# Optimization experiments

Measured on AMD Instinct MI355X. Metric: run time of the kernel, lower is better.

The kernel has to match this reference:

```python
import jax, jax.numpy as jnp
import numpy as np

# Model hyperparameters (match init_kwargs)
B, N_TOK, DIM = 32, 1024, 512
H_GRID, W_GRID = 32, 32
NT = 400
NUM_HEADS, KEY_DIM, ATTN_RATIO = 8, 64, 4
D_V = ATTN_RATIO * KEY_DIM          # 256, per-head value dim
DH = D_V * NUM_HEADS                # 2048
NH_KD = KEY_DIM * NUM_HEADS         # 512
H_KV = DH + NH_KD                   # 2560, kv projection width
NUM_OFFSETS = 100 * 100             # unique (|dx|,|dy|) offsets on 100x100 grid
EPS = 1e-5


def linear_bn(x, w, gamma, beta, mean, var):
    # Linear (no bias) followed by BatchNorm1d in inference form.
    y = x @ w
    return (y - mean) * (gamma * jax.lax.rsqrt(var + EPS)) + beta


def bias_idxs(H, W, nt):
    # attention_offsets[(a,b)] == a*100 + b (order of first-p1 sweep in __init__).
    # query n -> grid point (n//W, n%W); text token t -> (t//100, t%100).
    n = np.arange(H * W)
    i, j = n // W, n % W
    t = np.arange(nt)
    a, b = t // 100, t % 100
    return jnp.asarray(np.abs(i[:, None] - a[None, :]) * 100
                       + np.abs(j[:, None] - b[None, :]))  # (N, NT) int


def setup_inputs() -> dict:
    key = jax.random.key(0)
    ks = jax.random.split(key, 18)
    rn = jax.random.normal
    ru = jax.random.uniform
    return {
        "x": rn(ks[0], (B, N_TOK, DIM), jnp.float32),
        "text": rn(ks[1], (NT, DIM), jnp.float32),
        "q_w": rn(ks[2], (DIM, NH_KD), jnp.float32) * 0.02,
        "q_gamma": ru(ks[3], (NH_KD,), jnp.float32, 0.5, 1.5),
        "q_beta": rn(ks[4], (NH_KD,), jnp.float32) * 0.02,
        "q_mean": rn(ks[5], (NH_KD,), jnp.float32) * 0.02,
        "q_var": ru(ks[6], (NH_KD,), jnp.float32, 0.5, 1.5),
        "kv_w": rn(ks[7], (DIM, H_KV), jnp.float32) * 0.02,
        "kv_gamma": ru(ks[8], (H_KV,), jnp.float32, 0.5, 1.5),
        "kv_beta": rn(ks[9], (H_KV,), jnp.float32) * 0.02,
        "kv_mean": rn(ks[10], (H_KV,), jnp.float32) * 0.02,
        "kv_var": ru(ks[11], (H_KV,), jnp.float32, 0.5, 1.5),
        "proj_w": rn(ks[12], (DH, DIM), jnp.float32) * 0.02,
        "proj_gamma": ru(ks[13], (DIM,), jnp.float32, 0.5, 1.5),
        "proj_beta": rn(ks[14], (DIM,), jnp.float32) * 0.02,
        "proj_mean": rn(ks[15], (DIM,), jnp.float32) * 0.02,
        "proj_var": ru(ks[16], (DIM,), jnp.float32, 0.5, 1.5),
        "attention_biases": rn(ks[17], (NUM_HEADS, NUM_OFFSETS), jnp.float32) * 0.02,
        "H": H_GRID,
        "W": W_GRID,
    }


def reference(x, text, q_w, q_gamma, q_beta, q_mean, q_var,
              kv_w, kv_gamma, kv_beta, kv_mean, kv_var,
              proj_w, proj_gamma, proj_beta, proj_mean, proj_var,
              attention_biases, H, W):
    b, n, _ = x.shape
    nt = text.shape[0]
    scale = KEY_DIM ** -0.5

    # q: (B, heads, N, key_dim)
    q = linear_bn(x, q_w, q_gamma, q_beta, q_mean, q_var)
    q = q.reshape(b, n, NUM_HEADS, KEY_DIM).transpose(0, 2, 1, 3)

    # kv computed once on text, shared across batch: (NT, heads, key_dim + d)
    kv = linear_bn(text, kv_w, kv_gamma, kv_beta, kv_mean, kv_var)
    kv = kv.reshape(nt, NUM_HEADS, KEY_DIM + D_V)
    k, v = kv[:, :, :KEY_DIM], kv[:, :, KEY_DIM:]

    # gathered relative position bias: (heads, N, NT)
    idxs = bias_idxs(H, W, nt)
    bias = attention_biases[:, idxs]

    scores = jnp.einsum('bhnk,thk->bhnt', q, k) * scale + bias
    attn = jax.nn.softmax(scores, axis=-1)

    out = jnp.einsum('bhnt,thd->bhnd', attn, v)          # (B, heads, N, d)
    out = out.transpose(0, 2, 1, 3).reshape(b, n, DH)

    # proj = activation (GELU, exact) -> Linear_BN(dh -> dim)
    out = jax.nn.gelu(out, approximate=False)
    return linear_bn(out, proj_w, proj_gamma, proj_beta, proj_mean, proj_var)
```

## Files before the change

kernel.cpp:

```cpp
#include <hip/hip_runtime.h>
#include <hip/hip_bf16.h>


typedef unsigned short u16;
typedef unsigned int u32;
typedef float  f32x4  __attribute__((ext_vector_type(4)));
typedef float  fl4    __attribute__((ext_vector_type(4)));
typedef short  short8 __attribute__((ext_vector_type(8)));
typedef u32    u32x4  __attribute__((ext_vector_type(4)));
typedef u32    u32x2  __attribute__((ext_vector_type(2)));

#define EPSF 1e-5f
#define NH 8
#define NTP 416
#define LOG2E 1.4426950408889634f
#define QSCALE (0.125f * LOG2E)

static __device__ __forceinline__ u16 f2bf(float f){
  u32 u = __builtin_bit_cast(u32, f);
  u += 0x7FFFu + ((u >> 16) & 1u);
  return (u16)(u >> 16);
}
static __device__ __forceinline__ float u2f(u32 u){
  return __builtin_bit_cast(float, u);
}
static __device__ __forceinline__ u32 pk2bf(float lo, float hi){
  float2 f; f.x = lo; f.y = hi;
  __hip_bfloat162 b = __float22bfloat162_rn(f);
  u32 l = (u32)__bfloat16_as_ushort(b.x);
  u32 h = (u32)__bfloat16_as_ushort(b.y);
  return l | (h << 16);
}
static __device__ __forceinline__ f32x4 mfma16(short8 a, short8 b, f32x4 c){
  return __builtin_amdgcn_mfma_f32_16x16x32_bf16(a, b, c, 0, 0, 0);
}
static __device__ __forceinline__ void gld16(const void* g, void* l){
  __builtin_amdgcn_global_load_lds(
      (const __attribute__((address_space(1))) u32*)g,
      (__attribute__((address_space(3))) u32*)l, 16, 0, 0);
}

__global__ __launch_bounds__(256) void wconv_kernel(
    const float* __restrict__ w, const float* __restrict__ gamma,
    const float* __restrict__ var, u16* __restrict__ wT, int R, int C)
{
  __shared__ u16 tile[64*65];
  const int tx = blockIdx.x, ty = blockIdx.y, tid = threadIdx.x;
  #pragma unroll
  for (int i = 0; i < 16; ++i){
    int lin = tid + i*256;
    int rr = lin >> 6, cc = lin & 63;
    int c = tx*64 + cc;
    float s = gamma[c] * rsqrtf(var[c] + EPSF);
    tile[rr*65 + cc] = f2bf(w[(size_t)(ty*64 + rr)*C + c] * s);
  }
  __syncthreads();
  #pragma unroll
  for (int i = 0; i < 16; ++i){
    int lin = tid + i*256;
    int cc = lin >> 6, rr = lin & 63;
    wT[(size_t)(tx*64 + cc)*R + ty*64 + rr] = tile[rr*65 + cc];
  }
}

__global__ __launch_bounds__(256) void textconv_kernel(
    const float* __restrict__ text, u16* __restrict__ tbf)
{
  int idx = blockIdx.x*256 + threadIdx.x;
  int r = idx >> 9, c = idx & 511;
  float v = (r < 400) ? text[r*512 + c] : 0.f;
  tbf[idx] = f2bf(v);
}

__global__ __launch_bounds__(256) void bias_kernel(
    const float* __restrict__ ab, u16* __restrict__ btab)
{
  int idx = blockIdx.x*256 + threadIdx.x;
  int t = idx % 416;
  int n = (idx / 416) & 1023;
  int h = idx / (416*1024);
  float v;
  if (t >= 400) v = -1e30f;
  else {
    int i = n >> 5, j = n & 31;
    int a = t / 100, bb = t % 100;
    v = ab[h*10000 + abs(i - a)*100 + abs(j - bb)] * LOG2E;
  }
  size_t o = ((size_t)(h*16 + (n >> 6))*13 + (t >> 5))*2048
           + ((n >> 4) & 3)*512 + ((t >> 4) & 1)*256
           + ((t >> 2) & 3)*64 + (n & 15)*4 + (t & 3);
  btab[o] = f2bf(v);
}

template<int MODE, int NXB, int BK>
__global__ __launch_bounds__(256) void gemm_kernel(
    const void* __restrict__ Ap, const u16* __restrict__ BT,
    const float* __restrict__ g1, const float* __restrict__ b1,
    const float* __restrict__ m1, const float* __restrict__ v1,
    void* __restrict__ o0, void* __restrict__ o1, int K, int row_base,
    int rbpx)
{
  __shared__ u16 lds[BK == 64 ? 16384 : 8192];
  constexpr int HALF = (BK == 64) ? 8192 : 4096;
  const int tid = threadIdx.x;
  int cb, rb;
  if (NXB > 0){
    const int L = blockIdx.x;
    const int xcd = L & 7, s = L >> 3;
    cb = s % NXB;
    rb = xcd * rbpx + s / NXB;
  } else {
    cb = blockIdx.x; rb = blockIdx.y;
  }
  const int lane = tid & 63, wid = tid >> 6;
  const int lg = lane >> 4, lc = lane & 15;
  const int wr = wid >> 1, wc = wid & 1;
  const int row0 = rb*128, col0 = cb*128;
  f32x4 acc[4][4] = {};
  const int nkb = K / BK;

  for (int kb = 0; kb < nkb; ++kb){
    if (MODE == 0){
      const float* A = (const float*)Ap;
      #pragma unroll
      for (int it = 0; it < 4; ++it){
        int lin = tid + it*256;
        int row = lin >> 3, c4 = lin & 7;
        const fl4 v = *(const fl4*)(A + (size_t)(row0 + row)*K + kb*32 + c4*4);
        u32x2 p;
        p[0] = pk2bf(v[0], v[1]);
        p[1] = pk2bf(v[2], v[3]);
        *(u32x2*)&lds[row*32 + c4*4] = p;
      }
    } else if (BK == 32){
      const u16* A = (const u16*)Ap;
      #pragma unroll
      for (int it = 0; it < 2; ++it){
        int lin = tid + it*256;
        int row = lin >> 2, seg = lin & 3;
        gld16(A + (size_t)(row0 + row)*K + kb*32 + seg*8, &lds[lin*8]);
      }
    } else {
      const u16* A = (const u16*)Ap;
      #pragma unroll
      for (int it = 0; it < 4; ++it){
        int lin = tid + it*256;
        int row = lin >> 3, seg = lin & 7;
        gld16(A + (size_t)(row0 + row)*K + kb*64 + seg*8, &lds[lin*8]);
      }
    }
    if (BK == 32){
      #pragma unroll
      for (int it = 0; it < 2; ++it){
        int lin = tid + it*256;
        int col = lin >> 2, seg = lin & 3;
        gld16(BT + (size_t)(col0 + col)*K + kb*32 + seg*8, &lds[HALF + lin*8]);
      }
    } else {
      #pragma unroll
      for (int it = 0; it < 4; ++it){
        int lin = tid + it*256;
        int col = lin >> 3, seg = lin & 7;
        gld16(BT + (size_t)(col0 + col)*K + kb*64 + seg*8, &lds[HALF + lin*8]);
      }
    }
    __syncthreads();
    #pragma unroll
    for (int kh = 0; kh < BK/32; ++kh){
      short8 af[4], bfr[4];
      #pragma unroll
      for (int rt = 0; rt < 4; ++rt)
        af[rt] = *(const short8*)&lds[(wr*64 + rt*16 + lc)*BK + kh*32 + lg*8];
      #pragma unroll
      for (int ct = 0; ct < 4; ++ct)
        bfr[ct] = *(const short8*)&lds[HALF + (wc*64 + ct*16 + lc)*BK + kh*32 + lg*8];
      #pragma unroll
      for (int rt = 0; rt < 4; ++rt)
        #pragma unroll
        for (int ct = 0; ct < 4; ++ct)
          acc[rt][ct] = mfma16(af[rt], bfr[ct], acc[rt][ct]);
    }
    __syncthreads();
  }

  if (MODE == 0){
    u16* qws = (u16*)o0;
    #pragma unroll
    for (int ct = 0; ct < 4; ++ct){
      int c = col0 + wc*64 + ct*16 + lc;
      float sc = g1[c] * rsqrtf(v1[c] + EPSF);
      float sh = (b1[c] - m1[c]*sc) * QSCALE;
      int h = c >> 6, dk = c & 63;
      #pragma unroll
      for (int rt = 0; rt < 4; ++rt)
        #pragma unroll
        for (int r = 0; r < 4; ++r){
          int mr = row0 + wr*64 + rt*16 + lg*4 + r;
          int b = mr >> 10, n = mr & 1023;
          qws[(size_t)((b*NH + h)*1024 + n)*64 + dk] =
              f2bf(acc[rt][ct][r]*QSCALE + sh);
        }
    }
  } else if (MODE == 1){
    u16* Kw = (u16*)o0; u16* Vw = (u16*)o1;
    #pragma unroll
    for (int ct = 0; ct < 4; ++ct){
      int c = col0 + wc*64 + ct*16 + lc;
      float sc = g1[c] * rsqrtf(v1[c] + EPSF);
      float sh = b1[c] - m1[c]*sc;
      int h = c / 320, sub = c % 320;
      #pragma unroll
      for (int rt = 0; rt < 4; ++rt)
        #pragma unroll
        for (int r = 0; r < 4; ++r){
          int t = row0 + wr*64 + rt*16 + lg*4 + r;
          if (t < NTP){
            u16 val = f2bf(acc[rt][ct][r] + sh);
            if (sub < 64){
              size_t o = ((size_t)h*13 + (t >> 5))*2048
                       + ((t >> 4) & 1)*1024 + (sub >> 5)*512
                       + ((sub >> 3) & 3)*128 + (t & 15)*8 + (sub & 7);
              Kw[o] = val;
            } else {
              int dv = sub - 64;
              size_t o = ((size_t)h*13 + (t >> 5))*8192
                       + (dv >> 6)*2048 + ((dv >> 4) & 3)*512
                       + ((t >> 3) & 3)*128 + (dv & 15)*8 + (t & 7);
              Vw[o] = val;
            }
          }
        }
    }
  } else {
    float* outp = (float*)o0;
    #pragma unroll
    for (int ct = 0; ct < 4; ++ct){
      int c = col0 + wc*64 + ct*16 + lc;
      float sc = g1[c] * rsqrtf(v1[c] + EPSF);
      float sh = b1[c] - m1[c]*sc;
      #pragma unroll
      for (int rt = 0; rt < 4; ++rt)
        #pragma unroll
        for (int r = 0; r < 4; ++r){
          int mr = row_base + row0 + wr*64 + rt*16 + lg*4 + r;
          outp[(size_t)mr*512 + c] = acc[rt][ct][r] + sh;
        }
    }
  }
}

__global__ __launch_bounds__(256, 3) void attn_kernel(
    const u16* __restrict__ qws, const u16* __restrict__ Kw,
    const u16* __restrict__ Vw, const u16* __restrict__ btab,
    u16* __restrict__ aws, int b_base, int bzbits)
{
  __shared__ char Pb[2][64*80];
  __shared__ float lsum[64];

  const int tid = threadIdx.x;
  const int lane = tid & 63, wid = tid >> 6;
  const int lg = lane >> 4, lc = lane & 15;

  const int L = blockIdx.x;
  const int slot = L >> 3;
  const int bz = slot & ((1 << bzbits) - 1);
  const int qt = slot >> bzbits;
  const int h = L & 7;
  const int b = b_base + bz, n0 = qt*64;

  const u16* qp = qws + ((size_t)((b*NH + h)*1024 + n0 + wid*16 + lc))*64 + lg*8;
  const short8 qf0 = *(const short8*)qp;
  const short8 qf1 = *(const short8*)(qp + 32);

  const u16* kbase = Kw + (size_t)h*13*2048 + lg*128 + lc*8;
  const u16* vbase = Vw + (size_t)h*13*8192 + wid*2048 + lg*128 + lc*8;
  const u16* btb   = btab + ((size_t)(h*16 + qt)*13)*2048 + wid*512 + lg*64 + lc*4;

  float lpart = 0.f;
  f32x4 acc[4][4] = {};
  char* pwr = &Pb[0][0] + (wid*16 + lc)*80 + lg*8;

  short8 kfs[2][4];
  u32x2  bws[2][2];

  kfs[0][0] = *(const short8*)(kbase);
  kfs[0][1] = *(const short8*)(kbase + 512);
  kfs[0][2] = *(const short8*)(kbase + 1024);
  kfs[0][3] = *(const short8*)(kbase + 1536);
  bws[0][0] = *(const u32x2*)(btb);
  bws[0][1] = *(const u32x2*)(btb + 256);

  #pragma unroll
  for (int c = 0; c < 13; ++c){
    const int s = c & 1, ns = (c + 1) & 1;
    const u16* vc = vbase + (size_t)c*8192;
    short8 vf0 = *(const short8*)(vc);
    short8 vf1 = *(const short8*)(vc + 512);
    short8 vf2 = *(const short8*)(vc + 1024);
    short8 vf3 = *(const short8*)(vc + 1536);
    #pragma unroll
    for (int tt = 0; tt < 2; ++tt){
      u32x2 bw = bws[s][tt];
      f32x4 sv;
      sv[0] = u2f(bw[0] << 16); sv[1] = u2f(bw[0] & 0xffff0000u);
      sv[2] = u2f(bw[1] << 16); sv[3] = u2f(bw[1] & 0xffff0000u);
      sv = mfma16(kfs[s][tt*2 + 0], qf0, sv);
      sv = mfma16(kfs[s][tt*2 + 1], qf1, sv);
      float p0 = __builtin_exp2f(sv[0]);
      float p1 = __builtin_exp2f(sv[1]);
      float p2 = __builtin_exp2f(sv[2]);
      float p3 = __builtin_exp2f(sv[3]);
      lpart += (p0 + p1) + (p2 + p3);
      u32x2 pw;
      pw[0] = pk2bf(p0, p1);
      pw[1] = pk2bf(p2, p3);
      *(u32x2*)(pwr + s*5120 + tt*32) = pw;
    }
    if (c < 12){
      const u16* kc = kbase + (size_t)(c + 1)*2048;
      kfs[ns][0] = *(const short8*)(kc);
      kfs[ns][1] = *(const short8*)(kc + 512);
      kfs[ns][2] = *(const short8*)(kc + 1024);
      kfs[ns][3] = *(const short8*)(kc + 1536);
      const u16* bc = btb + (size_t)(c + 1)*2048;
      bws[ns][0] = *(const u32x2*)(bc);
      bws[ns][1] = *(const u32x2*)(bc + 256);
    }
    __syncthreads();
    const char* pb = &Pb[s][0];
    short8 pa[4];
    #pragma unroll
    for (int rt = 0; rt < 4; ++rt)
      pa[rt] = *(const short8*)(pb + (rt*16 + lc)*80 + lg*16);
    __builtin_amdgcn_s_setprio(1);
    #pragma unroll
    for (int rt = 0; rt < 4; ++rt){
      acc[rt][0] = mfma16(pa[rt], vf0, acc[rt][0]);
      acc[rt][1] = mfma16(pa[rt], vf1, acc[rt][1]);
      acc[rt][2] = mfma16(pa[rt], vf2, acc[rt][2]);
      acc[rt][3] = mfma16(pa[rt], vf3, acc[rt][3]);
    }
    __builtin_amdgcn_s_setprio(0);
  }

  lpart += __shfl_xor(lpart, 16);
  lpart += __shfl_xor(lpart, 32);
  if (lane < 16) lsum[wid*16 + lane] = lpart;
  __syncthreads();

  #pragma unroll
  for (int rt = 0; rt < 4; ++rt){
    #pragma unroll
    for (int r = 0; r < 4; ++r){
      const int qrow = rt*16 + lg*4 + r;
      const float linv = __builtin_amdgcn_rcpf(lsum[qrow]);
      const size_t obase = ((size_t)(bz*1024 + n0 + qrow))*2048 + h*256;
      #pragma unroll
      for (int ct = 0; ct < 4; ++ct){
        float x = acc[rt][ct][r] * linv;
        float x2 = x * x;
        float z = x * __builtin_fmaf(0.0356774081f, x2, 0.7978845608f);
        float e = __builtin_exp2f(z * (2.0f * LOG2E));
        float rr = __builtin_amdgcn_rcpf(1.0f + e);
        float g = __builtin_fmaf(-x, rr, x);
        aws[obase + wid*64 + ct*16 + lc] = f2bf(g);
      }
    }
  }
}

extern "C" void kernel_launch(void* const* d_in, const int* in_sizes, int n_in,
                              void* d_out, int out_size, void* d_ws, size_t ws_size,
                              hipStream_t stream)
{
  (void)in_sizes; (void)n_in; (void)out_size;
  const float* x    = (const float*)d_in[0];
  const float* text = (const float*)d_in[1];
  const float* q_w  = (const float*)d_in[2];
  const float* q_g  = (const float*)d_in[3];
  const float* q_b  = (const float*)d_in[4];
  const float* q_m  = (const float*)d_in[5];
  const float* q_v  = (const float*)d_in[6];
  const float* kv_w = (const float*)d_in[7];
  const float* kv_g = (const float*)d_in[8];
  const float* kv_b = (const float*)d_in[9];
  const float* kv_m = (const float*)d_in[10];
  const float* kv_v = (const float*)d_in[11];
  const float* p_w  = (const float*)d_in[12];
  const float* p_g  = (const float*)d_in[13];
  const float* p_b  = (const float*)d_in[14];
  const float* p_m  = (const float*)d_in[15];
  const float* p_v  = (const float*)d_in[16];
  const float* ab   = (const float*)d_in[17];
  float* out = (float*)d_out;

  char* ws = (char*)d_ws;
  u16* qwT   = (u16*)(ws + 0);
  u16* kvwT  = (u16*)(ws + 524288);
  u16* pwT   = (u16*)(ws + 3145728);
  u16* textb = (u16*)(ws + 5242880);
  u16* btab  = (u16*)(ws + 5767168);
  u16* Kw    = (u16*)(ws + 12582912);
  u16* Vw    = (u16*)(ws + 13008896);
  u16* qws   = (u16*)(ws + 14712832);
  u16* aws   = (u16*)(ws + 48267264);

  const bool full = ws_size >= (size_t)182484992ull;

  wconv_kernel<<<dim3(8, 8),  256, 0, stream>>>(q_w,  q_g,  q_v,  qwT,  512,  512);
  wconv_kernel<<<dim3(40, 8), 256, 0, stream>>>(kv_w, kv_g, kv_v, kvwT, 512,  2560);
  wconv_kernel<<<dim3(8, 32), 256, 0, stream>>>(p_w,  p_g,  p_v,  pwT,  2048, 512);
  textconv_kernel<<<1024, 256, 0, stream>>>(text, textb);
  bias_kernel<<<13312, 256, 0, stream>>>(ab, btab);

  gemm_kernel<1, 0, 32><<<dim3(20, 4), 256, 0, stream>>>(
      textb, kvwT, kv_g, kv_b, kv_m, kv_v, Kw, Vw, 512, 0, 0);
  gemm_kernel<0, 4, 32><<<1024, 256, 0, stream>>>(
      x, qwT, q_g, q_b, q_m, q_v, qws, nullptr, 512, 0, 32);

  if (full){
    attn_kernel<<<4096, 256, 0, stream>>>(qws, Kw, Vw, btab, aws, 0, 5);
    gemm_kernel<2, 4, 64><<<1024, 256, 0, stream>>>(
        aws, pwT, p_g, p_b, p_m, p_v, out, nullptr, 2048, 0, 32);
  } else {
    for (int q = 0; q < 4; ++q){
      attn_kernel<<<1024, 256, 0, stream>>>(qws, Kw, Vw, btab, aws, q*8, 3);
      gemm_kernel<2, 4, 64><<<256, 256, 0, stream>>>(
          aws, pwT, p_g, p_b, p_m, p_v, out, nullptr, 2048, q*8192, 8);
    }
  }
}
```

Before: 314.7 us.

## Add 256x256-tile double-buffered projection GEMM kernel for full-workspace path

Replaces the output-projection GEMM (32768x2048 @ 2048x512) in the full-workspace path with a new 512-thread kernel. It uses 256x256 output tiles, 128 KB of dynamic LDS with double-buffered direct global-to-LDS loads, XOR swizzling and s_setprio around the MFMA bursts. The larger tiles raise operand reuse and cut redundant reads of A and B compared with the previous 1024-block kernel. In exchange only 256 blocks launch with heavy LDS per block, which limits occupancy and latency hiding.

```diff
diff --git a/kernel.cpp b/kernel.cpp
--- a/kernel.cpp
+++ b/kernel.cpp
@@ -249,6 +249,103 @@
   }
 }
 
+__global__ __launch_bounds__(512, 2) void gemm256_kernel(
+    const u16* __restrict__ A, const u16* __restrict__ BT,
+    const float* __restrict__ g1, const float* __restrict__ b1,
+    const float* __restrict__ m1, const float* __restrict__ v1,
+    float* __restrict__ outp)
+{
+  extern __shared__ u16 lds[];
+  const int tid = threadIdx.x;
+  const int lane = tid & 63, wid = tid >> 6;
+  const int lg = lane >> 4, lc = lane & 15;
+  const int wm = wid >> 2, wn = wid & 3;
+
+  const int L = blockIdx.x;
+  const int xcd = L & 7, s = L >> 3;
+  const int cb = s & 1, rb = xcd*16 + (s >> 1);
+  const int row0 = rb*256, col0 = cb*256;
+
+  const int r0s = tid >> 3,  s0 = tid & 7;
+  const int r1s = (512 + tid) >> 3, s1 = (512 + tid) & 7;
+  const int ss0 = s0 ^ ((r0s & 4) >> 1);
+  const int ss1 = s1 ^ ((r1s & 4) >> 1);
+  const size_t aoff0 = (size_t)(row0 + r0s)*2048 + ss0*8;
+  const size_t aoff1 = (size_t)(row0 + r1s)*2048 + ss1*8;
+  const size_t boff0 = (size_t)(col0 + r0s)*2048 + ss0*8;
+  const size_t boff1 = (size_t)(col0 + r1s)*2048 + ss1*8;
+  const int d0 = tid*8, d1 = 4096 + tid*8;
+
+  auto stage = [&](int tk, int ht){
+    const int bb = (tk & 1) * 16384;
+    if (ht < 2){
+      gld16(A + aoff0 + (size_t)ht*262144 + tk*64, &lds[bb + ht*8192 + d0]);
+      gld16(A + aoff1 + (size_t)ht*262144 + tk*64, &lds[bb + ht*8192 + d1]);
+    } else {
+      const int h2 = ht - 2;
+      gld16(BT + boff0 + (size_t)h2*262144 + tk*64, &lds[32768 + bb + h2*8192 + d0]);
+      gld16(BT + boff1 + (size_t)h2*262144 + tk*64, &lds[32768 + bb + h2*8192 + d1]);
+    }
+  };
+
+  const int lgx = (lg*8) ^ ((lc & 4) << 2);
+  const int abase = wm*8192 + lc*64 + lgx;
+  const int bbase = 32768 + (wn >> 1)*8192 + ((wn & 1)*64 + lc)*64 + lgx;
+
+  f32x4 acc[8][4] = {};
+  short8 bf[4][2];
+
+  stage(0, 0); stage(0, 1); stage(0, 2); stage(0, 3);
+  asm volatile("s_waitcnt vmcnt(0)" ::: "memory");
+  __builtin_amdgcn_s_barrier();
+
+  for (int tk = 0; tk < 32; ++tk){
+    const int bc = (tk & 1) * 16384;
+    #pragma unroll
+    for (int p = 0; p < 4; ++p){
+      if (p == 0){
+        #pragma unroll
+        for (int cn = 0; cn < 4; ++cn){
+          bf[cn][0] = *(const short8*)&lds[bbase + bc + cn*1024];
+          bf[cn][1] = *(const short8*)&lds[bbase + bc + cn*1024 + 32];
+        }
+      }
+      short8 af[2][2];
+      #pragma unroll
+      for (int j = 0; j < 2; ++j){
+        af[j][0] = *(const short8*)&lds[abase + bc + (2*p + j)*1024];
+        af[j][1] = *(const short8*)&lds[abase + bc + (2*p + j)*1024 + 32];
+      }
+      if (tk < 31) stage(tk + 1, p);
+      if (p == 3) asm volatile("s_waitcnt vmcnt(0)" ::: "memory");
+      __builtin_amdgcn_s_barrier();
+      __builtin_amdgcn_s_setprio(1);
+      #pragma unroll
+      for (int j = 0; j < 2; ++j)
+        #pragma unroll
+        for (int cn = 0; cn < 4; ++cn){
+          acc[2*p + j][cn] = mfma16(af[j][0], bf[cn][0], acc[2*p + j][cn]);
+          acc[2*p + j][cn] = mfma16(af[j][1], bf[cn][1], acc[2*p + j][cn]);
+        }
+      __builtin_amdgcn_s_setprio(0);
+    }
+  }
+
+  #pragma unroll
+  for (int cn = 0; cn < 4; ++cn){
+    const int c = col0 + wn*64 + cn*16 + lc;
+    const float sc = g1[c] * rsqrtf(v1[c] + EPSF);
+    const float sh = b1[c] - m1[c]*sc;
+    #pragma unroll
+    for (int fr = 0; fr < 8; ++fr)
+      #pragma unroll
+      for (int r = 0; r < 4; ++r){
+        const int mr = row0 + wm*128 + fr*16 + lg*4 + r;
+        outp[(size_t)mr*512 + c] = acc[fr][cn][r] + sh;
+      }
+  }
+}
+
 __global__ __launch_bounds__(256, 3) void attn_kernel(
     const u16* __restrict__ qws, const u16* __restrict__ Kw,
     const u16* __restrict__ Vw, const u16* __restrict__ btab,
@@ -407,6 +504,9 @@
 
   const bool full = ws_size >= (size_t)182484992ull;
 
+  hipFuncSetAttribute((const void*)gemm256_kernel,
+                      hipFuncAttributeMaxDynamicSharedMemorySize, 131072);
+
   wconv_kernel<<<dim3(8, 8),  256, 0, stream>>>(q_w,  q_g,  q_v,  qwT,  512,  512);
   wconv_kernel<<<dim3(40, 8), 256, 0, stream>>>(kv_w, kv_g, kv_v, kvwT, 512,  2560);
   wconv_kernel<<<dim3(8, 32), 256, 0, stream>>>(p_w,  p_g,  p_v,  pwT,  2048, 512);
@@ -420,8 +520,8 @@
 
   if (full){
     attn_kernel<<<4096, 256, 0, stream>>>(qws, Kw, Vw, btab, aws, 0, 5);
-    gemm_kernel<2, 4, 64><<<1024, 256, 0, stream>>>(
-        aws, pwT, p_g, p_b, p_m, p_v, out, nullptr, 2048, 0, 32);
+    gemm256_kernel<<<256, 512, 131072, stream>>>(
+        aws, pwT, p_g, p_b, p_m, p_v, out);
   } else {
     for (int q = 0; q < 4; ++q){
       attn_kernel<<<1024, 256, 0, stream>>>(qws, Kw, Vw, btab, aws, q*8, 3);
```

Result: faster. 292.4 us (-7.1%).
